# Kernel optimization log

Measured on AMD Instinct MI355X. Metric: run time of the kernel, lower is better.

The kernel has to match this reference:

```python
import jax, jax.numpy as jnp
import numpy as np

B, S, UNITS = 32, 2048, 512

def setup_inputs() -> dict:
    key = jax.random.key(0)
    ks = jax.random.split(key, 8)
    sc = 1.0 / np.sqrt(UNITS)
    return {
        "s_prev": jax.random.normal(ks[0], (B, UNITS), jnp.float32),
        "hidden_states": jax.random.normal(ks[1], (B, S, UNITS), jnp.float32),
        "W_kernel": jax.random.normal(ks[2], (UNITS, UNITS), jnp.float32) * sc,
        "W_bias": jnp.zeros((UNITS,), jnp.float32),
        "U_kernel": jax.random.normal(ks[3], (UNITS, UNITS), jnp.float32) * sc,
        "U_bias": jnp.zeros((UNITS,), jnp.float32),
        "V_kernel": jax.random.normal(ks[4], (UNITS, 1), jnp.float32) * sc,
        "V_bias": jnp.zeros((1,), jnp.float32),
    }

def reference(s_prev, hidden_states, W_kernel, W_bias, U_kernel, U_bias, V_kernel, V_bias):
    # NOTE: faithful to the source code: U is applied to s_prev, W to hidden_states,
    # and the context is computed as softmax-weights * s_prev (as written, a quirk
    # of the original module), summed over the sequence axis.
    first = s_prev @ U_kernel + U_bias                      # (B, units)
    second = hidden_states @ W_kernel + W_bias              # (B, S, units)
    score = jnp.tanh(first[:, None, :] + second) @ V_kernel + V_bias  # (B, S, 1)
    weights = jax.nn.softmax(score, axis=1)                 # (B, S, 1)
    context = jnp.sum(weights * s_prev[:, None, :], axis=1) # (B, units)
    return context, weights
```

## Files before the change

kernel.cpp:

```cpp
#include <hip/hip_runtime.h>

#define NBATCH 32
#define SEQ    2048
#define NU     512
#define ASTR   36

typedef __attribute__((ext_vector_type(8)))  short bf16x8;
typedef __attribute__((ext_vector_type(16))) float f32x16;

__device__ __forceinline__ short bf16_rne(float f) {
  union { float f; unsigned u; } v; v.f = f;
  unsigned r = v.u + 0x7fffu + ((v.u >> 16) & 1u);
  return (short)(r >> 16);
}

__device__ __forceinline__ unsigned pk2(float lo, float hi) {
  return __builtin_amdgcn_perm(__float_as_uint(hi), __float_as_uint(lo), 0x07060302u);
}

__device__ __forceinline__ float fast_tanh(float x) {
  float ax = __builtin_fabsf(x);
  float t  = __expf(-2.0f * ax);
  float r  = (1.0f - t) / (1.0f + t);
  return x < 0.0f ? -r : r;
}

__global__ __launch_bounds__(256) void prep_all(const float* __restrict__ W,
                                                const float* __restrict__ sp,
                                                const float* __restrict__ U,
                                                const float* __restrict__ Ub,
                                                const float* __restrict__ Wb,
                                                short* __restrict__ Wt,
                                                float* __restrict__ first) {
  __shared__ float srow[NU];
  if (blockIdx.x < 1024) {
    int idx = blockIdx.x * 256 + threadIdx.x;
    int u = idx >> 9, k = idx & 511;
    Wt[(size_t)u * NU + k] = bf16_rne(W[(size_t)k * NU + u]);
  } else {
    int blk = blockIdx.x - 1024;
    int b = blk >> 1, half = blk & 1, t = threadIdx.x;
    srow[t]       = sp[b * NU + t];
    srow[t + 256] = sp[b * NU + t + 256];
    __syncthreads();
    int col = half * 256 + t;
    float acc = Ub[col] + Wb[col];
    #pragma unroll 8
    for (int k = 0; k < NU; ++k) acc += srow[k] * U[(size_t)k * NU + col];
    first[b * NU + col] = acc;
  }
}

__global__ __launch_bounds__(512, 4) void attn_main(
    const float* __restrict__ h,
    const short* __restrict__ Wt,
    const float* __restrict__ first,
    const float* __restrict__ V,
    float* __restrict__ s0)
{
  __shared__ short Alds[2][256 * ASTR];
  __shared__ short Blds[2][128 * ASTR];
  __shared__ float scores_lds[256];

  const int tid  = threadIdx.x;
  const int lane = tid & 63;
  const int w    = tid >> 6;
  const int wr   = w >> 1, wc = w & 1;
  const int l31  = lane & 31, hi = lane >> 5;

  const int bid = blockIdx.x;
  const int lb  = (bid & 7) * 128 + (bid >> 3);
  const int panel = lb >> 2, q = lb & 3;
  const int rowbase = panel * 256;
  const int b = panel >> 3;

  const int arow  = tid >> 1;
  const int ahalf = tid & 1;
  const float* hA = h + (size_t)(rowbase + arow) * NU + ahalf * 16;
  const int awr   = arow * ASTR + ahalf * 16;
  const short* bsrc = Wt + (size_t)(q * 128 + (tid >> 2)) * NU + (tid & 3) * 8;
  const int bwr   = (tid >> 2) * ASTR + (tid & 3) * 8;

  const int rA0 = (wr * 64 + l31) * ASTR + hi * 8;
  const int rA1 = rA0 + 32 * ASTR;
  const int rB0 = (wc * 64 + l31) * ASTR + hi * 8;
  const int rB1 = rB0 + 32 * ASTR;

  f32x16 acc[2][2];
  #pragma unroll
  for (int rt = 0; rt < 2; ++rt)
    #pragma unroll
    for (int ct = 0; ct < 2; ++ct)
      #pragma unroll
      for (int r = 0; r < 16; ++r) acc[rt][ct][r] = 0.f;

  float4 ha0, ha1, ha2, ha3;
  float4 hb0, hb1, hb2, hb3;
  int4   bqa, bqb;

  #define LOAD_H(V0, V1, V2, V3, ktn)                                       \
    {                                                                       \
      const float* p = hA + (ktn) * 32;                                     \
      V0 = *reinterpret_cast<const float4*>(p + 0);                         \
      V1 = *reinterpret_cast<const float4*>(p + 4);                         \
      V2 = *reinterpret_cast<const float4*>(p + 8);                         \
      V3 = *reinterpret_cast<const float4*>(p + 12);                        \
    }

  #define CVT_WRITE(dst, V0, V1, V2, V3, BQ)                                \
    {                                                                       \
      uint4 u0, u1;                                                         \
      u0.x = pk2(V0.x, V0.y); u0.y = pk2(V0.z, V0.w);                       \
      u0.z = pk2(V1.x, V1.y); u0.w = pk2(V1.z, V1.w);                       \
      u1.x = pk2(V2.x, V2.y); u1.y = pk2(V2.z, V2.w);                       \
      u1.z = pk2(V3.x, V3.y); u1.w = pk2(V3.z, V3.w);                       \
      *reinterpret_cast<uint4*>(&Alds[dst][awr])     = u0;                  \
      *reinterpret_cast<uint4*>(&Alds[dst][awr + 8]) = u1;                  \
      *reinterpret_cast<int4*>(&Blds[dst][bwr])      = BQ;                  \
    }

  #define COMPUTE(cur)                                                      \
    _Pragma("unroll")                                                       \
    for (int ks = 0; ks < 2; ++ks) {                                        \
      bf16x8 af0, af1, bf0, bf1;                                            \
      af0 = *reinterpret_cast<const bf16x8*>(&Alds[cur][rA0 + ks * 16]);    \
      af1 = *reinterpret_cast<const bf16x8*>(&Alds[cur][rA1 + ks * 16]);    \
      bf0 = *reinterpret_cast<const bf16x8*>(&Blds[cur][rB0 + ks * 16]);    \
      bf1 = *reinterpret_cast<const bf16x8*>(&Blds[cur][rB1 + ks * 16]);    \
      acc[0][0] = __builtin_amdgcn_mfma_f32_32x32x16_bf16(af0, bf0, acc[0][0], 0, 0, 0); \
      acc[0][1] = __builtin_amdgcn_mfma_f32_32x32x16_bf16(af0, bf1, acc[0][1], 0, 0, 0); \
      acc[1][0] = __builtin_amdgcn_mfma_f32_32x32x16_bf16(af1, bf0, acc[1][0], 0, 0, 0); \
      acc[1][1] = __builtin_amdgcn_mfma_f32_32x32x16_bf16(af1, bf1, acc[1][1], 0, 0, 0); \
    }

  #define BAR_LGKM                                                          \
    asm volatile("s_waitcnt lgkmcnt(0)" ::: "memory");                      \
    __builtin_amdgcn_s_barrier();                                           \
    asm volatile("" ::: "memory");

  bqa = *reinterpret_cast<const int4*>(bsrc);
  LOAD_H(ha0, ha1, ha2, ha3, 0);
  CVT_WRITE(0, ha0, ha1, ha2, ha3, bqa);
  bqb = *reinterpret_cast<const int4*>(bsrc + 1 * 32);
  LOAD_H(hb0, hb1, hb2, hb3, 1);
  BAR_LGKM;

  #pragma unroll 1
  for (int kt2 = 0; kt2 < 6; ++kt2) {
    const int kt = kt2 * 2;
    bqa = *reinterpret_cast<const int4*>(bsrc + (kt + 2) * 32);
    LOAD_H(ha0, ha1, ha2, ha3, kt + 2);
    COMPUTE(0);
    CVT_WRITE(1, hb0, hb1, hb2, hb3, bqb);
    BAR_LGKM;
    bqb = *reinterpret_cast<const int4*>(bsrc + (kt + 3) * 32);
    LOAD_H(hb0, hb1, hb2, hb3, kt + 3);
    COMPUTE(1);
    CVT_WRITE(0, ha0, ha1, ha2, ha3, bqa);
    BAR_LGKM;
  }

  bqa = *reinterpret_cast<const int4*>(bsrc + 14 * 32);
  LOAD_H(ha0, ha1, ha2, ha3, 14);
  COMPUTE(0);
  CVT_WRITE(1, hb0, hb1, hb2, hb3, bqb);
  BAR_LGKM;

  bqb = *reinterpret_cast<const int4*>(bsrc + 15 * 32);
  LOAD_H(hb0, hb1, hb2, hb3, 15);
  COMPUTE(1);
  CVT_WRITE(0, ha0, ha1, ha2, ha3, bqa);
  BAR_LGKM;

  COMPUTE(0);
  CVT_WRITE(1, hb0, hb1, hb2, hb3, bqb);
  BAR_LGKM;

  COMPUTE(1);

  #undef LOAD_H
  #undef CVT_WRITE
  #undef COMPUTE
  #undef BAR_LGKM

  float fv[2], vv[2];
  #pragma unroll
  for (int ct = 0; ct < 2; ++ct) {
    int col = q * 128 + wc * 64 + ct * 32 + l31;
    fv[ct] = first[b * NU + col];
    vv[ct] = V[col];
  }
  float part[2][16];
  #pragma unroll
  for (int rt = 0; rt < 2; ++rt) {
    #pragma unroll
    for (int r = 0; r < 16; ++r) {
      float p = 0.f;
      #pragma unroll
      for (int ct = 0; ct < 2; ++ct)
        p += vv[ct] * fast_tanh(fv[ct] + acc[rt][ct][r]);
      #pragma unroll
      for (int m = 1; m < 32; m <<= 1) p += __shfl_xor(p, m, 64);
      part[rt][r] = p;
    }
  }
  __syncthreads();
  if (wc == 0 && l31 == 0) {
    #pragma unroll
    for (int rt = 0; rt < 2; ++rt)
      #pragma unroll
      for (int r = 0; r < 16; ++r)
        scores_lds[wr * 64 + rt * 32 + (r & 3) + 8 * (r >> 2) + 4 * hi] = part[rt][r];
  }
  __syncthreads();
  if (wc == 1 && l31 == 0) {
    #pragma unroll
    for (int rt = 0; rt < 2; ++rt)
      #pragma unroll
      for (int r = 0; r < 16; ++r)
        scores_lds[wr * 64 + rt * 32 + (r & 3) + 8 * (r >> 2) + 4 * hi] += part[rt][r];
  }
  __syncthreads();
  if (tid < 256) atomicAdd(&s0[rowbase + tid], scores_lds[tid]);
}

__global__ __launch_bounds__(256) void softmax_ctx(const float* __restrict__ sp,
                                                   float* __restrict__ out) {
  const int b = blockIdx.x;
  const int t = threadIdx.x;
  float* wgt = out + NBATCH * NU + (size_t)b * SEQ;
  __shared__ float red[4];

  float v[8];
  float mx = -1e30f;
  #pragma unroll
  for (int i = 0; i < 8; ++i) { v[i] = wgt[t + i * 256]; mx = fmaxf(mx, v[i]); }
  #pragma unroll
  for (int m = 1; m < 64; m <<= 1) mx = fmaxf(mx, __shfl_xor(mx, m, 64));
  if ((t & 63) == 0) red[t >> 6] = mx;
  __syncthreads();
  mx = fmaxf(fmaxf(red[0], red[1]), fmaxf(red[2], red[3]));
  __syncthreads();

  float se = 0.f;
  #pragma unroll
  for (int i = 0; i < 8; ++i) { v[i] = __expf(v[i] - mx); se += v[i]; }
  #pragma unroll
  for (int m = 1; m < 64; m <<= 1) se += __shfl_xor(se, m, 64);
  if ((t & 63) == 0) red[t >> 6] = se;
  __syncthreads();
  se = red[0] + red[1] + red[2] + red[3];
  __syncthreads();

  const float inv = 1.0f / se;
  float sw = 0.f;
  #pragma unroll
  for (int i = 0; i < 8; ++i) { float wi = v[i] * inv; wgt[t + i * 256] = wi; sw += wi; }
  #pragma unroll
  for (int m = 1; m < 64; m <<= 1) sw += __shfl_xor(sw, m, 64);
  if ((t & 63) == 0) red[t >> 6] = sw;
  __syncthreads();
  sw = red[0] + red[1] + red[2] + red[3];

  out[b * NU + t]       = sp[b * NU + t] * sw;
  out[b * NU + t + 256] = sp[b * NU + t + 256] * sw;
}

extern "C" void kernel_launch(void* const* d_in, const int* in_sizes, int n_in,
                              void* d_out, int out_size, void* d_ws, size_t ws_size,
                              hipStream_t stream) {
  (void)in_sizes; (void)n_in; (void)out_size; (void)ws_size;
  const float* s_prev = (const float*)d_in[0];
  const float* h      = (const float*)d_in[1];
  const float* Wk     = (const float*)d_in[2];
  const float* Wb     = (const float*)d_in[3];
  const float* Uk     = (const float*)d_in[4];
  const float* Ub     = (const float*)d_in[5];
  const float* Vk     = (const float*)d_in[6];

  float* out   = (float*)d_out;
  float* first = (float*)d_ws;
  short* Wt    = (short*)((char*)d_ws + 65536);
  float* s0    = out + NBATCH * NU;

  hipMemsetAsync(s0, 0, (size_t)NBATCH * SEQ * sizeof(float), stream);
  prep_all   <<<1088, 256, 0, stream>>>(Wk, s_prev, Uk, Ub, Wb, Wt, first);
  attn_main  <<<1024, 512, 0, stream>>>(h, Wt, first, Vk, s0);
  softmax_ctx<<<  32, 256, 0, stream>>>(s_prev, out);
}
```

Measured before the change: 111.5 us.

## Pre-swizzle W into MFMA fragment layout and load B operands directly to registers

The prep kernel now writes W as bf16 in the exact per-lane MFMA B-fragment order, so the main kernel loads B fragments straight from global memory into registers instead of staging them through LDS. This removes the B tile from shared memory, along with its LDS writes and reads, and cuts the prep grid from 1088 to 192 blocks. MFMA issue is wrapped in s_setprio to favour the matrix core. In exchange the main kernel needs more registers for the double-buffered fragments, and each wave now fetches its own B data from L2 rather than sharing one LDS copy within the block.

```diff
diff --git a/kernel.cpp b/kernel.cpp
--- a/kernel.cpp
+++ b/kernel.cpp
@@ -30,15 +30,21 @@
                                                 const float* __restrict__ U,
                                                 const float* __restrict__ Ub,
                                                 const float* __restrict__ Wb,
-                                                short* __restrict__ Wt,
+                                                short* __restrict__ Wfrag,
                                                 float* __restrict__ first) {
   __shared__ float srow[NU];
-  if (blockIdx.x < 1024) {
+  if (blockIdx.x < 128) {
     int idx = blockIdx.x * 256 + threadIdx.x;
-    int u = idx >> 9, k = idx & 511;
-    Wt[(size_t)u * NU + k] = bf16_rne(W[(size_t)k * NU + u]);
+    int l = idx & 63;
+    int s = (idx >> 6) & 31;
+    int g = idx >> 11;
+    int colg = g * 32 + (l & 31);
+    int kbase = s * 16 + ((l >> 5) << 3);
+    #pragma unroll
+    for (int j = 0; j < 8; ++j)
+      Wfrag[(size_t)idx * 8 + j] = bf16_rne(W[(size_t)(kbase + j) * NU + colg]);
   } else {
-    int blk = blockIdx.x - 1024;
+    int blk = blockIdx.x - 128;
     int b = blk >> 1, half = blk & 1, t = threadIdx.x;
     srow[t]       = sp[b * NU + t];
     srow[t + 256] = sp[b * NU + t + 256];
@@ -53,13 +59,12 @@
 
 __global__ __launch_bounds__(512, 4) void attn_main(
     const float* __restrict__ h,
-    const short* __restrict__ Wt,
+    const short* __restrict__ Wfrag,
     const float* __restrict__ first,
     const float* __restrict__ V,
     float* __restrict__ s0)
 {
   __shared__ short Alds[2][256 * ASTR];
-  __shared__ short Blds[2][128 * ASTR];
   __shared__ float scores_lds[256];
 
   const int tid  = threadIdx.x;
@@ -78,13 +83,13 @@
   const int ahalf = tid & 1;
   const float* hA = h + (size_t)(rowbase + arow) * NU + ahalf * 16;
   const int awr   = arow * ASTR + ahalf * 16;
-  const short* bsrc = Wt + (size_t)(q * 128 + (tid >> 2)) * NU + (tid & 3) * 8;
-  const int bwr   = (tid >> 2) * ASTR + (tid & 3) * 8;
+
+  const int g0 = q * 4 + wc * 2;
+  const bf16x8* wf0 = reinterpret_cast<const bf16x8*>(Wfrag) + (size_t)g0 * 32 * 64 + lane;
+  const bf16x8* wf1 = wf0 + 32 * 64;
 
   const int rA0 = (wr * 64 + l31) * ASTR + hi * 8;
   const int rA1 = rA0 + 32 * ASTR;
-  const int rB0 = (wc * 64 + l31) * ASTR + hi * 8;
-  const int rB1 = rB0 + 32 * ASTR;
 
   f32x16 acc[2][2];
   #pragma unroll
@@ -96,7 +101,8 @@
 
   float4 ha0, ha1, ha2, ha3;
   float4 hb0, hb1, hb2, hb3;
-  int4   bqa, bqb;
+  bf16x8 fa00, fa01, fa10, fa11;
+  bf16x8 fb00, fb01, fb10, fb11;
 
   #define LOAD_H(V0, V1, V2, V3, ktn)                                       \
     {                                                                       \
@@ -107,7 +113,15 @@
       V3 = *reinterpret_cast<const float4*>(p + 12);                        \
     }
 
-  #define CVT_WRITE(dst, V0, V1, V2, V3, BQ)                                \
+  #define LOAD_F(F00, F01, F10, F11, ktn)                                   \
+    {                                                                       \
+      F00 = wf0[(size_t)(2 * (ktn) + 0) * 64];                              \
+      F01 = wf0[(size_t)(2 * (ktn) + 1) * 64];                              \
+      F10 = wf1[(size_t)(2 * (ktn) + 0) * 64];                              \
+      F11 = wf1[(size_t)(2 * (ktn) + 1) * 64];                              \
+    }
+
+  #define CVT_WRITE(dst, V0, V1, V2, V3)                                    \
     {                                                                       \
       uint4 u0, u1;                                                         \
       u0.x = pk2(V0.x, V0.y); u0.y = pk2(V0.z, V0.w);                       \
@@ -116,21 +130,25 @@
       u1.z = pk2(V3.x, V3.y); u1.w = pk2(V3.z, V3.w);                       \
       *reinterpret_cast<uint4*>(&Alds[dst][awr])     = u0;                  \
       *reinterpret_cast<uint4*>(&Alds[dst][awr + 8]) = u1;                  \
-      *reinterpret_cast<int4*>(&Blds[dst][bwr])      = BQ;                  \
-    }
-
-  #define COMPUTE(cur)                                                      \
-    _Pragma("unroll")                                                       \
-    for (int ks = 0; ks < 2; ++ks) {                                        \
-      bf16x8 af0, af1, bf0, bf1;                                            \
-      af0 = *reinterpret_cast<const bf16x8*>(&Alds[cur][rA0 + ks * 16]);    \
-      af1 = *reinterpret_cast<const bf16x8*>(&Alds[cur][rA1 + ks * 16]);    \
-      bf0 = *reinterpret_cast<const bf16x8*>(&Blds[cur][rB0 + ks * 16]);    \
-      bf1 = *reinterpret_cast<const bf16x8*>(&Blds[cur][rB1 + ks * 16]);    \
-      acc[0][0] = __builtin_amdgcn_mfma_f32_32x32x16_bf16(af0, bf0, acc[0][0], 0, 0, 0); \
-      acc[0][1] = __builtin_amdgcn_mfma_f32_32x32x16_bf16(af0, bf1, acc[0][1], 0, 0, 0); \
-      acc[1][0] = __builtin_amdgcn_mfma_f32_32x32x16_bf16(af1, bf0, acc[1][0], 0, 0, 0); \
-      acc[1][1] = __builtin_amdgcn_mfma_f32_32x32x16_bf16(af1, bf1, acc[1][1], 0, 0, 0); \
+    }
+
+  #define COMPUTE(cur, F00, F01, F10, F11)                                  \
+    {                                                                       \
+      bf16x8 af0, af1, ag0, ag1;                                            \
+      af0 = *reinterpret_cast<const bf16x8*>(&Alds[cur][rA0]);              \
+      af1 = *reinterpret_cast<const bf16x8*>(&Alds[cur][rA1]);              \
+      ag0 = *reinterpret_cast<const bf16x8*>(&Alds[cur][rA0 + 16]);         \
+      ag1 = *reinterpret_cast<const bf16x8*>(&Alds[cur][rA1 + 16]);         \
+      __builtin_amdgcn_s_setprio(1);                                        \
+      acc[0][0] = __builtin_amdgcn_mfma_f32_32x32x16_bf16(af0, F00, acc[0][0], 0, 0, 0); \
+      acc[0][1] = __builtin_amdgcn_mfma_f32_32x32x16_bf16(af0, F10, acc[0][1], 0, 0, 0); \
+      acc[1][0] = __builtin_amdgcn_mfma_f32_32x32x16_bf16(af1, F00, acc[1][0], 0, 0, 0); \
+      acc[1][1] = __builtin_amdgcn_mfma_f32_32x32x16_bf16(af1, F10, acc[1][1], 0, 0, 0); \
+      acc[0][0] = __builtin_amdgcn_mfma_f32_32x32x16_bf16(ag0, F01, acc[0][0], 0, 0, 0); \
+      acc[0][1] = __builtin_amdgcn_mfma_f32_32x32x16_bf16(ag0, F11, acc[0][1], 0, 0, 0); \
+      acc[1][0] = __builtin_amdgcn_mfma_f32_32x32x16_bf16(ag1, F01, acc[1][0], 0, 0, 0); \
+      acc[1][1] = __builtin_amdgcn_mfma_f32_32x32x16_bf16(ag1, F11, acc[1][1], 0, 0, 0); \
+      __builtin_amdgcn_s_setprio(0);                                        \
     }
 
   #define BAR_LGKM                                                          \
@@ -138,47 +156,48 @@
     __builtin_amdgcn_s_barrier();                                           \
     asm volatile("" ::: "memory");
 
-  bqa = *reinterpret_cast<const int4*>(bsrc);
   LOAD_H(ha0, ha1, ha2, ha3, 0);
-  CVT_WRITE(0, ha0, ha1, ha2, ha3, bqa);
-  bqb = *reinterpret_cast<const int4*>(bsrc + 1 * 32);
+  CVT_WRITE(0, ha0, ha1, ha2, ha3);
   LOAD_H(hb0, hb1, hb2, hb3, 1);
+  LOAD_F(fa00, fa01, fa10, fa11, 0);
+  LOAD_F(fb00, fb01, fb10, fb11, 1);
   BAR_LGKM;
 
   #pragma unroll 1
   for (int kt2 = 0; kt2 < 6; ++kt2) {
     const int kt = kt2 * 2;
-    bqa = *reinterpret_cast<const int4*>(bsrc + (kt + 2) * 32);
     LOAD_H(ha0, ha1, ha2, ha3, kt + 2);
-    COMPUTE(0);
-    CVT_WRITE(1, hb0, hb1, hb2, hb3, bqb);
+    COMPUTE(0, fa00, fa01, fa10, fa11);
+    LOAD_F(fa00, fa01, fa10, fa11, kt + 2);
+    CVT_WRITE(1, hb0, hb1, hb2, hb3);
     BAR_LGKM;
-    bqb = *reinterpret_cast<const int4*>(bsrc + (kt + 3) * 32);
     LOAD_H(hb0, hb1, hb2, hb3, kt + 3);
-    COMPUTE(1);
-    CVT_WRITE(0, ha0, ha1, ha2, ha3, bqa);
+    COMPUTE(1, fb00, fb01, fb10, fb11);
+    LOAD_F(fb00, fb01, fb10, fb11, kt + 3);
+    CVT_WRITE(0, ha0, ha1, ha2, ha3);
     BAR_LGKM;
   }
 
-  bqa = *reinterpret_cast<const int4*>(bsrc + 14 * 32);
   LOAD_H(ha0, ha1, ha2, ha3, 14);
-  COMPUTE(0);
-  CVT_WRITE(1, hb0, hb1, hb2, hb3, bqb);
+  COMPUTE(0, fa00, fa01, fa10, fa11);
+  LOAD_F(fa00, fa01, fa10, fa11, 14);
+  CVT_WRITE(1, hb0, hb1, hb2, hb3);
   BAR_LGKM;
 
-  bqb = *reinterpret_cast<const int4*>(bsrc + 15 * 32);
   LOAD_H(hb0, hb1, hb2, hb3, 15);
-  COMPUTE(1);
-  CVT_WRITE(0, ha0, ha1, ha2, ha3, bqa);
+  COMPUTE(1, fb00, fb01, fb10, fb11);
+  LOAD_F(fb00, fb01, fb10, fb11, 15);
+  CVT_WRITE(0, ha0, ha1, ha2, ha3);
   BAR_LGKM;
 
-  COMPUTE(0);
-  CVT_WRITE(1, hb0, hb1, hb2, hb3, bqb);
+  COMPUTE(0, fa00, fa01, fa10, fa11);
+  CVT_WRITE(1, hb0, hb1, hb2, hb3);
   BAR_LGKM;
 
-  COMPUTE(1);
+  COMPUTE(1, fb00, fb01, fb10, fb11);
 
   #undef LOAD_H
+  #undef LOAD_F
   #undef CVT_WRITE
   #undef COMPUTE
   #undef BAR_LGKM
@@ -280,11 +299,11 @@
 
   float* out   = (float*)d_out;
   float* first = (float*)d_ws;
-  short* Wt    = (short*)((char*)d_ws + 65536);
+  short* Wfrag = (short*)((char*)d_ws + 65536);
   float* s0    = out + NBATCH * NU;
 
   hipMemsetAsync(s0, 0, (size_t)NBATCH * SEQ * sizeof(float), stream);
-  prep_all   <<<1088, 256, 0, stream>>>(Wk, s_prev, Uk, Ub, Wb, Wt, first);
-  attn_main  <<<1024, 512, 0, stream>>>(h, Wt, first, Vk, s0);
+  prep_all   <<< 192, 256, 0, stream>>>(Wk, s_prev, Uk, Ub, Wb, Wfrag, first);
+  attn_main  <<<1024, 512, 0, stream>>>(h, Wfrag, first, Vk, s0);
   softmax_ctx<<<  32, 256, 0, stream>>>(s_prev, out);
 }
```

Result: slower. 272.8 us (+144.6%).
